# Optimization experiments

Measured on AMD Instinct MI355X. Metric: run time of the kernel, lower is better.

## Reference

```python
import jax, jax.numpy as jnp
import numpy as np

B, S, H, NH = 2, 2048, 768, 12
HD = H // NH
MEM_W = 0.5  # memory_weight
LN_EPS = 1e-5


def setup_inputs() -> dict:
    key = jax.random.key(0)
    ks = jax.random.split(key, 12)
    xav = lambda k: jax.random.uniform(k, (H, H), jnp.float32, -1.0, 1.0) * np.sqrt(6.0 / (H + H))
    return {
        "hidden_states": jax.random.normal(ks[0], (B, S, H), jnp.float32),
        "cross_states": jax.random.normal(ks[1], (B, S, H), jnp.float32),
        "attention_mask": jnp.ones((B, 1, S, S), jnp.int32),
        "memory_tensors": jax.random.normal(ks[2], (2, B, S, H), jnp.float32),
        "dynamic_factor": jax.random.uniform(ks[3], (B, S, 1), jnp.float32),
        "Wq": xav(ks[4]), "bq": jnp.zeros((H,), jnp.float32),
        "Wk": xav(ks[5]), "bk": jnp.zeros((H,), jnp.float32),
        "Wv": xav(ks[6]), "bv": jnp.zeros((H,), jnp.float32),
        "Wo": xav(ks[7]), "bo": jnp.zeros((H,), jnp.float32),
        "gate": jnp.ones((1,), jnp.float32),
        "gate_bias": jnp.zeros((1,), jnp.float32),
        "ln_g": jnp.ones((H,), jnp.float32),
        "ln_b": jnp.zeros((H,), jnp.float32),
    }


def _layernorm(x, g, b):
    mu = jnp.mean(x, axis=-1, keepdims=True)
    var = jnp.mean(jnp.square(x - mu), axis=-1, keepdims=True)
    return (x - mu) * jax.lax.rsqrt(var + LN_EPS) * g + b


def reference(hidden_states, cross_states, attention_mask, memory_tensors,
              dynamic_factor, Wq, bq, Wk, bk, Wv, bv, Wo, bo,
              gate, gate_bias, ln_g, ln_b):
    x = _layernorm(hidden_states, ln_g, ln_b)
    q = x @ Wq + bq                      # [B,S,H]
    k = cross_states @ Wk + bk
    v = cross_states @ Wv + bv
    k = k + memory_tensors[0] * MEM_W    # memory injection into K/V
    v = v + memory_tensors[1] * MEM_W

    q = q.reshape(B, S, NH, HD).transpose(0, 2, 1, 3)  # [B,NH,S,HD]
    k = k.reshape(B, S, NH, HD).transpose(0, 2, 1, 3)
    v = v.reshape(B, S, NH, HD).transpose(0, 2, 1, 3)

    scores = jnp.einsum("bhqd,bhkd->bhqk", q, k) / np.sqrt(HD)
    scores = jnp.where(attention_mask == 0, -jnp.inf, scores)
    attn = jax.nn.softmax(scores, axis=-1)
    out = jnp.einsum("bhqk,bhkd->bhqd", attn, v)       # [B,NH,S,HD]
    out = out.transpose(0, 2, 1, 3).reshape(B, S, H)

    out = out @ Wo + bo
    out = out * gate + gate_bias
    out = out * dynamic_factor
    return out
```

## Files before the change

### kernel.cpp

```cpp
#include <hip/hip_runtime.h>
#include <hip/hip_bf16.h>
#include <stdint.h>

#define BB   2
#define SS   2048
#define HH   768
#define NHH  12
#define HDD  64
#define BSS  (BB*SS)
#define NBH  (BB*NHH)
#define ROWS_BH (NBH*SS)
#define NSPLIT 2

typedef unsigned short u16;
typedef unsigned int   u32;
typedef __attribute__((ext_vector_type(8))) short bf16x8_t;
typedef __attribute__((ext_vector_type(4))) float f32x4;
typedef __attribute__((ext_vector_type(16))) float f32x16;
typedef __attribute__((ext_vector_type(2))) u32   u32x2;
typedef __attribute__((ext_vector_type(4))) u32   u32x4;

#define MFMA16(a, b, c) __builtin_amdgcn_mfma_f32_16x16x32_bf16((a), (b), (c), 0, 0, 0)
#define MFMA32(a, b, c) __builtin_amdgcn_mfma_f32_32x32x16_bf16((a), (b), (c), 0, 0, 0)

__device__ __forceinline__ float b2f(u16 u) {
    u32 x = ((u32)u) << 16; float f; __builtin_memcpy(&f, &x, 4); return f;
}
__device__ __forceinline__ u16 f2b(float f) {
    u32 x; __builtin_memcpy(&x, &f, 4);
    u32 r = x + 0x7fffu + ((x >> 16) & 1u);
    return (u16)(r >> 16);
}
__device__ __forceinline__ u32 cvtpk(float a, float b) {
    u32 r;
    __asm__("v_cvt_pk_bf16_f32 %0, %1, %2" : "=v"(r) : "v"(a), "v"(b));
    return r;
}
__device__ __forceinline__ void async16(const u16* g, u16* l) {
    __builtin_amdgcn_global_load_lds(
        (const __attribute__((address_space(1))) void*)g,
        (__attribute__((address_space(3))) void*)l, 16, 0, 0);
}

__global__ __launch_bounds__(256) void prep_kernel(
    const float* __restrict__ Wq, const float* __restrict__ Wk,
    const float* __restrict__ Wv, const float* __restrict__ Wo,
    u16* __restrict__ Wt,
    const float* __restrict__ hid, const float* __restrict__ cross,
    const float* __restrict__ g, const float* __restrict__ bb,
    u16* __restrict__ xln, u16* __restrict__ crossb,
    const int* __restrict__ mask, u32* __restrict__ bits,
    u32* __restrict__ wrow)
{
    int id = blockIdx.x;
    int t = threadIdx.x;

    if (id < 576) {
        int mat = id / 144, rem = id % 144;
        int by = rem / 12, bx = rem % 12;
        const float* src = (mat == 0) ? Wq : (mat == 1) ? Wk : (mat == 2) ? Wv : Wo;
        u16* dst = Wt + (size_t)mat * 768 * 768;

        __shared__ float sm[64][68];
        int r0 = by * 64, c0 = bx * 64;
        #pragma unroll
        for (int it = 0; it < 4; ++it) {
            int c = t + it * 256;
            int r = c >> 4, sg = c & 15;
            *(float4*)&sm[r][sg * 4] = *(const float4*)&src[(size_t)(r0 + r) * 768 + c0 + sg * 4];
        }
        __syncthreads();
        #pragma unroll
        for (int it = 0; it < 2; ++it) {
            int c = t + it * 256;
            int rr = c >> 3, sg = c & 7;
            u16 tmp[8] __attribute__((aligned(16)));
            #pragma unroll
            for (int j = 0; j < 8; ++j) tmp[j] = f2b(sm[sg * 8 + j][rr]);
            *(u32x4*)&dst[(size_t)(c0 + rr) * 768 + r0 + sg * 8] = *(u32x4*)tmp;
        }
        return;
    }

    if (id < 2624) {
        int lid = id - 576;
        int y = lid >> 10, bx = lid & 1023;
        int wv = t >> 6, lane = t & 63;
        int row = bx * 4 + wv;

        if (y == 1) {
            const float* xr = cross + (size_t)row * 768;
            u16* o = crossb + (size_t)row * 768;
            #pragma unroll
            for (int c = 0; c < 3; ++c) {
                float4 f = *(const float4*)&xr[c * 256 + lane * 4];
                u16 t4[4] __attribute__((aligned(8)));
                t4[0] = f2b(f.x); t4[1] = f2b(f.y); t4[2] = f2b(f.z); t4[3] = f2b(f.w);
                *(u32x2*)&o[c * 256 + lane * 4] = *(u32x2*)t4;
            }
            return;
        }

        const float* xr = hid + (size_t)row * 768;
        float v[12];
        float s = 0.f, s2 = 0.f;
        #pragma unroll
        for (int c = 0; c < 3; ++c) {
            float4 f = *(const float4*)&xr[c * 256 + lane * 4];
            v[c*4+0] = f.x; v[c*4+1] = f.y; v[c*4+2] = f.z; v[c*4+3] = f.w;
            s  += f.x + f.y + f.z + f.w;
            s2 += f.x*f.x + f.y*f.y + f.z*f.z + f.w*f.w;
        }
        #pragma unroll
        for (int off = 1; off < 64; off <<= 1) {
            s  += __shfl_xor(s,  off, 64);
            s2 += __shfl_xor(s2, off, 64);
        }
        float mu  = s  * (1.f / 768.f);
        float var = s2 * (1.f / 768.f) - mu * mu;
        float rs  = 1.f / sqrtf(var + 1e-5f);
        #pragma unroll
        for (int c = 0; c < 3; ++c) {
            float4 gg = *(const float4*)&g [c * 256 + lane * 4];
            float4 bv = *(const float4*)&bb[c * 256 + lane * 4];
            u16 o[4] __attribute__((aligned(8)));
            o[0] = f2b((v[c*4+0] - mu) * rs * gg.x + bv.x);
            o[1] = f2b((v[c*4+1] - mu) * rs * gg.y + bv.y);
            o[2] = f2b((v[c*4+2] - mu) * rs * gg.z + bv.z);
            o[3] = f2b((v[c*4+3] - mu) * rs * gg.w + bv.w);
            *(u32x2*)&xln[(size_t)row * 768 + c * 256 + lane * 4] = *(u32x2*)o;
        }
        return;
    }

    {
        int mid = id - 2624;
        int w = mid * 256 + t;
        const int4* p = (const int4*)(mask + (size_t)w * 32);
        u32 v = 0;
        #pragma unroll
        for (int i = 0; i < 8; ++i) {
            int4 m = p[i];
            v |= ((m.x != 0) ? 1u : 0u) << (4 * i + 0);
            v |= ((m.y != 0) ? 1u : 0u) << (4 * i + 1);
            v |= ((m.z != 0) ? 1u : 0u) << (4 * i + 2);
            v |= ((m.w != 0) ? 1u : 0u) << (4 * i + 3);
        }
        bits[w] = v;
        unsigned long long ball = __ballot(v == 0xffffffffu);
        if ((t & 63) == 0) {
            u32 wr = 0;
            #pragma unroll
            for (int kt = 0; kt < 32; ++kt)
                if (((ball >> (2 * kt)) & 3ull) == 3ull) wr |= (1u << kt);
            wrow[w >> 6] = wr;
        }
    }
}

__device__ __forceinline__ void gemm64_main(const u16* __restrict__ A,
                                            const u16* __restrict__ W,
                                            f32x4 acc[2][4])
{
    __shared__ __attribute__((aligned(16))) u16 AsL[64 * 64];
    __shared__ __attribute__((aligned(16))) u16 BsL[128 * 64];
    int m0 = blockIdx.x * 64, n0 = blockIdx.y * 128;
    int t = threadIdx.x;
    int wv = t >> 6, lane = t & 63, lm = lane & 15, quad = lane >> 4;
    int wr = wv >> 1, wc = wv & 1;

    for (int kt = 0; kt < 768 / 64; ++kt) {
        __syncthreads();
        #pragma unroll
        for (int it = 0; it < 2; ++it) {
            int c = t + it * 256;
            int row = c >> 3, cs = (c & 7) ^ (row & 7);
            async16(A + (size_t)(m0 + row) * 768 + kt * 64 + cs * 8, &AsL[c * 8]);
        }
        #pragma unroll
        for (int it = 0; it < 4; ++it) {
            int c = t + it * 256;
            int row = c >> 3, cs = (c & 7) ^ (row & 7);
            async16(W + (size_t)(n0 + row) * 768 + kt * 64 + cs * 8, &BsL[c * 8]);
        }
        __syncthreads();
        #pragma unroll
        for (int kk = 0; kk < 2; ++kk) {
            bf16x8_t af[2], bfv[4];
            #pragma unroll
            for (int i = 0; i < 2; ++i) {
                int r = wr * 32 + i * 16 + lm;
                af[i] = *(const bf16x8_t*)&AsL[(r * 8 + ((kk * 4 + quad) ^ (r & 7))) * 8];
            }
            #pragma unroll
            for (int j = 0; j < 4; ++j) {
                int r = wc * 64 + j * 16 + lm;
                bfv[j] = *(const bf16x8_t*)&BsL[(r * 8 + ((kk * 4 + quad) ^ (r & 7))) * 8];
            }
            #pragma unroll
            for (int i = 0; i < 2; ++i)
                #pragma unroll
                for (int j = 0; j < 4; ++j)
                    acc[i][j] = MFMA16(af[i], bfv[j], acc[i][j]);
        }
    }
}

__global__ __launch_bounds__(256) void qkv_gemm(
    const u16* __restrict__ xln, const u16* __restrict__ crossb,
    const u16* __restrict__ Wt,  const float* __restrict__ bq,
    const float* __restrict__ bk, const float* __restrict__ bv,
    const float* __restrict__ mem,
    u16* __restrict__ Qb, u16* __restrict__ Kb, u16* __restrict__ VtG)
{
    int z = blockIdx.z;
    const u16* A      = (z == 0) ? xln : crossb;
    const u16* W      = Wt + (size_t)z * 768 * 768;
    const float* bias = (z == 0) ? bq : (z == 1) ? bk : bv;
    const float* mp   = (z == 0) ? (const float*)nullptr : mem + (size_t)(z - 1) * BSS * HH;

    f32x4 z4 = {0.f, 0.f, 0.f, 0.f};
    f32x4 acc[2][4];
    #pragma unroll
    for (int i = 0; i < 2; ++i)
        #pragma unroll
        for (int j = 0; j < 4; ++j) acc[i][j] = z4;

    gemm64_main(A, W, acc);

    int t = threadIdx.x, wv = t >> 6, lane = t & 63, lm = lane & 15, quad = lane >> 4;
    int wr = wv >> 1, wc = wv & 1;
    int row0 = blockIdx.x * 64 + wr * 32 + quad * 4;
    int col0 = blockIdx.y * 128 + wc * 64 + lm;

    if (z == 2) {
        #pragma unroll
        for (int j = 0; j < 4; ++j) {
            int cg = col0 + j * 16;
            float bz = bias[cg];
            int h = cg >> 6, d = cg & 63;
            #pragma unroll
            for (int i = 0; i < 2; ++i) {
                int rg = row0 + i * 16;
                int b = rg >> 11, s = rg & 2047;
                u16 ob[4] __attribute__((aligned(8)));
                #pragma unroll
                for (int e = 0; e < 4; ++e) {
                    float v = acc[i][j][e] + bz + 0.5f * mp[(size_t)(rg + e) * HH + cg];
                    ob[e] = f2b(v);
                }
                *(u32x2*)&VtG[((size_t)(b * NHH + h) * 64 + d) * SS + s] = *(u32x2*)ob;
            }
        }
        return;
    }

    u16* out = (z == 0) ? Qb : Kb;
    #pragma unroll
    for (int j = 0; j < 4; ++j) {
        int cg = col0 + j * 16;
        float bz = bias[cg];
        #pragma unroll
        for (int i = 0; i < 2; ++i) {
            int rg = row0 + i * 16;
            #pragma unroll
            for (int e = 0; e < 4; ++e) {
                float v = acc[i][j][e] + bz;
                if (mp) v += 0.5f * mp[(size_t)(rg + e) * HH + cg];
                out[(size_t)(rg + e) * HH + cg] = f2b(v);
            }
        }
    }
}

__global__ __launch_bounds__(256, 3) void attn_kernel(
    const u16* __restrict__ Q, const u16* __restrict__ K,
    const u16* __restrict__ VtG, const u32* __restrict__ mbits,
    const u32* __restrict__ wrow,
    u16* __restrict__ Pacc, float* __restrict__ Pl, int ksteps)
{
    __shared__ __attribute__((aligned(16))) u16 KsL[2][64 * 64];
    __shared__ __attribute__((aligned(16))) u16 VtL[2][64 * 64];

    int qt = blockIdx.x;
    int bh = blockIdx.y;
    int z  = blockIdx.z;
    int b = bh / NHH, h = bh % NHH;
    int t = threadIdx.x;
    int wv = t >> 6, lane = t & 63;
    int q31 = lane & 31, hi = lane >> 5;

    int qbase = qt * 128 + wv * 32;
    const u16* qp = Q + (size_t)(b * SS + qbase + q31) * HH + h * 64 + hi * 8;
    bf16x8_t qf0 = *(const bf16x8_t*)&qp[0];
    bf16x8_t qf1 = *(const bf16x8_t*)&qp[16];
    bf16x8_t qf2 = *(const bf16x8_t*)&qp[32];
    bf16x8_t qf3 = *(const bf16x8_t*)&qp[48];

    f32x16 acc0 = {};
    f32x16 acc1 = {};
    float l_lane = 0.f;

    const float SC = 0.18033688011112042f;

    u32 wl = wrow[b * SS + qbase + q31];
    const u32* mrow = &mbits[(size_t)(b * SS + qbase + q31) * (SS / 32)];

    int kr = t >> 3, cs = (t & 7) ^ (kr & 7);
    const u16* Kb0 = K + (size_t)(b * SS) * HH + h * 64;
    const u16* Vb0 = VtG + (size_t)bh * 64 * SS;

    auto STAGE = [&](int pp, int kt) {
        int k0 = kt * 64;
        #pragma unroll
        for (int it = 0; it < 2; ++it) {
            int c = t + it * 256;
            int rr = c >> 3, ss = (c & 7) ^ (rr & 7);
            async16(Kb0 + (size_t)(k0 + rr) * HH + ss * 8, &KsL[pp][c * 8]);
            async16(Vb0 + (size_t)rr * SS + k0 + ss * 8,   &VtL[pp][c * 8]);
        }
    };
    (void)kr; (void)cs;

    int kt0 = z * ksteps, ktE = kt0 + ksteps;
    STAGE(0, kt0);
    __syncthreads();

    for (int kt = kt0; kt < ktE; ++kt) {
        int p = (kt - kt0) & 1;
        if (kt + 1 < ktE) STAGE(p ^ 1, kt + 1);

        bool ok = __all((int)((wl >> kt) & 1u));
        unsigned long long mw = ~0ull;
        if (!ok) {
            u32x2 u = *(const u32x2*)&mrow[kt * 2];
            mw = ((unsigned long long)u.y << 32) | (unsigned long long)u.x;
        }

        #pragma unroll
        for (int kb = 0; kb < 2; ++kb) {
            f32x16 sc = {};
            #pragma unroll
            for (int step = 0; step < 4; ++step) {
                int row = kb * 32 + q31;
                int ch = (step * 2 + hi) ^ (row & 7);
                bf16x8_t kf = *(const bf16x8_t*)&KsL[p][(row * 8 + ch) * 8];
                bf16x8_t qf = (step == 0) ? qf0 : (step == 1) ? qf1 : (step == 2) ? qf2 : qf3;
                sc = MFMA32(kf, qf, sc);
            }

            #pragma unroll
            for (int r = 0; r < 16; ++r) {
                float pv = __builtin_amdgcn_exp2f(sc[r] * SC);
                if (!ok) {
                    int kbit = kb * 32 + (r & 3) + 8 * (r >> 2) + 4 * hi;
                    if (!((mw >> kbit) & 1ull)) pv = 0.f;
                }
                sc[r] = pv;
                l_lane += pv;
            }

            #pragma unroll
            for (int s2 = 0; s2 < 2; ++s2) {
                u32 P0 = cvtpk(sc[8 * s2 + 0], sc[8 * s2 + 1]);
                u32 P1 = cvtpk(sc[8 * s2 + 2], sc[8 * s2 + 3]);
                u32 P2 = cvtpk(sc[8 * s2 + 4], sc[8 * s2 + 5]);
                u32 P3 = cvtpk(sc[8 * s2 + 6], sc[8 * s2 + 7]);
                auto s02 = __builtin_amdgcn_permlane32_swap((int)P0, (int)P2, false, false);
                auto s13 = __builtin_amdgcn_permlane32_swap((int)P1, (int)P3, false, false);
                u32x4 w;
                w.x = (u32)s02[0]; w.y = (u32)s13[0];
                w.z = (u32)s02[1]; w.w = (u32)s13[1];
                bf16x8_t pf = __builtin_bit_cast(bf16x8_t, w);

                int vrow0 = q31;
                int vrow1 = 32 + q31;
                int ch = kb * 4 + s2 * 2 + hi;
                bf16x8_t vf0 = *(const bf16x8_t*)&VtL[p][(vrow0 * 8 + (ch ^ (vrow0 & 7))) * 8];
                bf16x8_t vf1 = *(const bf16x8_t*)&VtL[p][(vrow1 * 8 + (ch ^ (vrow1 & 7))) * 8];
                acc0 = MFMA32(pf, vf0, acc0);
                acc1 = MFMA32(pf, vf1, acc1);
            }
        }

        __syncthreads();
    }

    l_lane += __shfl_xor(l_lane, 32, 64);

    size_t prow0 = ((size_t)z * NBH + bh) * SS + qt * 128 + wv * 32;
    #pragma unroll
    for (int r = 0; r < 16; ++r) {
        int qrow = (r & 3) + 8 * (r >> 2) + 4 * hi;
        Pacc[(prow0 + qrow) * 64 + q31]      = f2b(acc0[r]);
        Pacc[(prow0 + qrow) * 64 + 32 + q31] = f2b(acc1[r]);
    }
    if (lane < 32) Pl[prow0 + lane] = l_lane;
}

__global__ __launch_bounds__(256) void attn_merge(
    const u16* __restrict__ Pacc, const float* __restrict__ Pl,
    u16* __restrict__ AO)
{
    int t = threadIdx.x;
    int r = blockIdx.x * 64 + (t >> 2);
    int dseg = (t & 3) * 16;

    float lsum = Pl[r] + Pl[(size_t)ROWS_BH + r];

    float o[16];
    #pragma unroll
    for (int i = 0; i < 16; ++i) o[i] = 0.f;
    #pragma unroll
    for (int s = 0; s < NSPLIT; ++s) {
        const u16* ap = &Pacc[((size_t)s * ROWS_BH + r) * 64 + dseg];
        u32x4 a0 = *(const u32x4*)ap;
        u32x4 a1 = *(const u32x4*)(ap + 8);
        u32 wa[8];
        wa[0]=a0.x; wa[1]=a0.y; wa[2]=a0.z; wa[3]=a0.w;
        wa[4]=a1.x; wa[5]=a1.y; wa[6]=a1.z; wa[7]=a1.w;
        #pragma unroll
        for (int i = 0; i < 8; ++i) {
            o[2*i]   += b2f((u16)(wa[i] & 0xffff));
            o[2*i+1] += b2f((u16)(wa[i] >> 16));
        }
    }
    float inv = 1.f / lsum;
    int bh = r >> 11, q = r & 2047;
    int b = bh / NHH, h = bh % NHH;
    u16 ob[16] __attribute__((aligned(16)));
    #pragma unroll
    for (int i = 0; i < 16; ++i) ob[i] = f2b(o[i] * inv);
    u16* op = &AO[((size_t)(b * SS + q)) * HH + h * 64 + dseg];
    *(u32x4*)op       = *(u32x4*)ob;
    *(u32x4*)(op + 8) = *(u32x4*)(ob + 8);
}

__global__ __launch_bounds__(256) void out_gemm(
    const u16* __restrict__ AO, const u16* __restrict__ Wt,
    const float* __restrict__ bo, const float* __restrict__ gate,
    const float* __restrict__ gbias, const float* __restrict__ dyn,
    float* __restrict__ out)
{
    f32x4 z4 = {0.f, 0.f, 0.f, 0.f};
    f32x4 acc[2][4];
    #pragma unroll
    for (int i = 0; i < 2; ++i)
        #pragma unroll
        for (int j = 0; j < 4; ++j) acc[i][j] = z4;

    gemm64_main(AO, Wt, acc);

    float gv = gate[0];
    float gb = gbias[0];
    int t = threadIdx.x, wv = t >> 6, lane = t & 63, lm = lane & 15, quad = lane >> 4;
    int wr = wv >> 1, wc = wv & 1;
    int row0 = blockIdx.x * 64 + wr * 32 + quad * 4;
    int col0 = blockIdx.y * 128 + wc * 64 + lm;
    #pragma unroll
    for (int j = 0; j < 4; ++j) {
        int cg = col0 + j * 16;
        float bz = bo[cg];
        #pragma unroll
        for (int i = 0; i < 2; ++i) {
            int rg = row0 + i * 16;
            #pragma unroll
            for (int e = 0; e < 4; ++e) {
                float v = acc[i][j][e] + bz;
                v = v * gv + gb;
                v *= dyn[rg + e];
                out[(size_t)(rg + e) * HH + cg] = v;
            }
        }
    }
}

extern "C" void kernel_launch(void* const* d_in, const int* in_sizes, int n_in,
                              void* d_out, int out_size, void* d_ws, size_t ws_size,
                              hipStream_t stream)
{
    (void)in_sizes; (void)n_in; (void)out_size; (void)ws_size;

    const float* hid   = (const float*)d_in[0];
    const float* cross = (const float*)d_in[1];
    const int*   amask = (const int*)d_in[2];
    const float* mem   = (const float*)d_in[3];
    const float* dyn   = (const float*)d_in[4];
    const float* Wq    = (const float*)d_in[5];
    const float* bq    = (const float*)d_in[6];
    const float* Wk    = (const float*)d_in[7];
    const float* bk    = (const float*)d_in[8];
    const float* Wv    = (const float*)d_in[9];
    const float* bv    = (const float*)d_in[10];
    const float* Wo    = (const float*)d_in[11];
    const float* bo    = (const float*)d_in[12];
    const float* gate  = (const float*)d_in[13];
    const float* gbias = (const float*)d_in[14];
    const float* lng   = (const float*)d_in[15];
    const float* lnb   = (const float*)d_in[16];

    char* p = (char*)d_ws;
    u16* Wt   = (u16*)p; p += (size_t)4 * 768 * 768 * 2;
    u32* mb   = (u32*)p; p += (size_t)BB * SS * (SS / 32) * 4;
    u32* wrow = (u32*)p; p += (size_t)BSS * 4;
    u16* xln  = (u16*)p; p += (size_t)BSS * HH * 2;
    u16* crb  = (u16*)p; p += (size_t)BSS * HH * 2;
    u16* Qb   = (u16*)p; p += (size_t)BSS * HH * 2;
    u16* Kb   = (u16*)p; p += (size_t)BSS * HH * 2;
    u16* VtG  = (u16*)p; p += (size_t)BSS * HH * 2;
    u16* Pacc  = xln;
    float* Pl  = (float*)Wt;
    u16* AO    = Kb;

    prep_kernel <<<dim3(3648),           256, 0, stream>>>(
        Wq, Wk, Wv, Wo, Wt, hid, cross, lng, lnb, xln, crb, amask, mb, wrow);
    qkv_gemm    <<<dim3(64, 6, 3),       256, 0, stream>>>(
        xln, crb, Wt, bq, bk, bv, mem, Qb, Kb, VtG);
    attn_kernel <<<dim3(16, 24, NSPLIT), 256, 0, stream>>>(
        Qb, Kb, VtG, mb, wrow, Pacc, Pl, SS / 64 / NSPLIT);
    attn_merge  <<<dim3(ROWS_BH / 64),   256, 0, stream>>>(Pacc, Pl, AO);
    out_gemm    <<<dim3(64, 6),          256, 0, stream>>>(
        AO, Wt + (size_t)3 * 768 * 768, bo, gate, gbias, dyn, (float*)d_out);
}
```

Baseline: 238.7 us.

## Triple-buffer attention K/V loads and remap block IDs for XCD locality

The attention kernel moves from double to triple buffering of K/V tiles. It uses explicit vmcnt waits and a single barrier per step, and the compile-time k-loop is fully unrolled, so loads run two tiles ahead of compute. All three GEMM/attention kernels switch to a 1-D grid with a block-ID swizzle `(bid&7)*N + bid>>3`. This places neighbouring logical tiles on the same XCD to improve L2 reuse. In exchange, LDS per block grows, which may lower occupancy, and the hand-written waitcnt counts depend on how many loads each stage issues.

```diff
diff --git a/kernel.cpp b/kernel.cpp
--- a/kernel.cpp
+++ b/kernel.cpp
@@ -11,6 +11,7 @@
 #define NBH  (BB*NHH)
 #define ROWS_BH (NBH*SS)
 #define NSPLIT 2
+#define KST  (SS / 64 / NSPLIT)
 
 typedef unsigned short u16;
 typedef unsigned int   u32;
@@ -160,11 +161,11 @@
 
 __device__ __forceinline__ void gemm64_main(const u16* __restrict__ A,
                                             const u16* __restrict__ W,
+                                            int m0, int n0,
                                             f32x4 acc[2][4])
 {
     __shared__ __attribute__((aligned(16))) u16 AsL[64 * 64];
     __shared__ __attribute__((aligned(16))) u16 BsL[128 * 64];
-    int m0 = blockIdx.x * 64, n0 = blockIdx.y * 128;
     int t = threadIdx.x;
     int wv = t >> 6, lane = t & 63, lm = lane & 15, quad = lane >> 4;
     int wr = wv >> 1, wc = wv & 1;
@@ -213,7 +214,13 @@
     const float* __restrict__ mem,
     u16* __restrict__ Qb, u16* __restrict__ Kb, u16* __restrict__ VtG)
 {
-    int z = blockIdx.z;
+    int bid = blockIdx.x;
+    int logical = (bid & 7) * 144 + (bid >> 3);
+    int bx = logical & 63;
+    int rest = logical >> 6;
+    int by = rest % 6;
+    int z  = rest / 6;
+
     const u16* A      = (z == 0) ? xln : crossb;
     const u16* W      = Wt + (size_t)z * 768 * 768;
     const float* bias = (z == 0) ? bq : (z == 1) ? bk : bv;
@@ -226,12 +233,12 @@
         #pragma unroll
         for (int j = 0; j < 4; ++j) acc[i][j] = z4;
 
-    gemm64_main(A, W, acc);
+    gemm64_main(A, W, bx * 64, by * 128, acc);
 
     int t = threadIdx.x, wv = t >> 6, lane = t & 63, lm = lane & 15, quad = lane >> 4;
     int wr = wv >> 1, wc = wv & 1;
-    int row0 = blockIdx.x * 64 + wr * 32 + quad * 4;
-    int col0 = blockIdx.y * 128 + wc * 64 + lm;
+    int row0 = bx * 64 + wr * 32 + quad * 4;
+    int col0 = by * 128 + wc * 64 + lm;
 
     if (z == 2) {
         #pragma unroll
@@ -277,14 +284,18 @@
     const u16* __restrict__ Q, const u16* __restrict__ K,
     const u16* __restrict__ VtG, const u32* __restrict__ mbits,
     const u32* __restrict__ wrow,
-    u16* __restrict__ Pacc, float* __restrict__ Pl, int ksteps)
-{
-    __shared__ __attribute__((aligned(16))) u16 KsL[2][64 * 64];
-    __shared__ __attribute__((aligned(16))) u16 VtL[2][64 * 64];
-
-    int qt = blockIdx.x;
-    int bh = blockIdx.y;
-    int z  = blockIdx.z;
+    u16* __restrict__ Pacc, float* __restrict__ Pl)
+{
+    __shared__ __attribute__((aligned(16))) u16 KsL[3][64 * 64];
+    __shared__ __attribute__((aligned(16))) u16 VtL[3][64 * 64];
+
+    int bid = blockIdx.x;
+    int logical = (bid & 7) * 96 + (bid >> 3);
+    int qt = logical & 15;
+    int g  = logical >> 4;
+    int bh = g >> 1;
+    int z  = g & 1;
+
     int b = bh / NHH, h = bh % NHH;
     int t = threadIdx.x;
     int wv = t >> 6, lane = t & 63;
@@ -306,7 +317,6 @@
     u32 wl = wrow[b * SS + qbase + q31];
     const u32* mrow = &mbits[(size_t)(b * SS + qbase + q31) * (SS / 32)];
 
-    int kr = t >> 3, cs = (t & 7) ^ (kr & 7);
     const u16* Kb0 = K + (size_t)(b * SS) * HH + h * 64;
     const u16* Vb0 = VtG + (size_t)bh * 64 * SS;
 
@@ -320,15 +330,25 @@
             async16(Vb0 + (size_t)rr * SS + k0 + ss * 8,   &VtL[pp][c * 8]);
         }
     };
-    (void)kr; (void)cs;
-
-    int kt0 = z * ksteps, ktE = kt0 + ksteps;
+
+    int kt0 = z * KST;
     STAGE(0, kt0);
-    __syncthreads();
-
-    for (int kt = kt0; kt < ktE; ++kt) {
-        int p = (kt - kt0) & 1;
-        if (kt + 1 < ktE) STAGE(p ^ 1, kt + 1);
+    __builtin_amdgcn_sched_barrier(0);
+    STAGE(1, kt0 + 1);
+    __builtin_amdgcn_sched_barrier(0);
+
+    #pragma unroll
+    for (int i = 0; i < KST; ++i) {
+        int kt = kt0 + i;
+        int cur = i % 3;
+
+        if (i + 1 < KST) { __asm__ volatile("s_waitcnt vmcnt(4)" ::: "memory"); }
+        else             { __asm__ volatile("s_waitcnt vmcnt(0)" ::: "memory"); }
+        __builtin_amdgcn_s_barrier();
+        __builtin_amdgcn_sched_barrier(0);
+
+        if (i + 2 < KST) STAGE((i + 2) % 3, kt + 2);
+        __builtin_amdgcn_sched_barrier(0);
 
         bool ok = __all((int)((wl >> kt) & 1u));
         unsigned long long mw = ~0ull;
@@ -344,7 +364,7 @@
             for (int step = 0; step < 4; ++step) {
                 int row = kb * 32 + q31;
                 int ch = (step * 2 + hi) ^ (row & 7);
-                bf16x8_t kf = *(const bf16x8_t*)&KsL[p][(row * 8 + ch) * 8];
+                bf16x8_t kf = *(const bf16x8_t*)&KsL[cur][(row * 8 + ch) * 8];
                 bf16x8_t qf = (step == 0) ? qf0 : (step == 1) ? qf1 : (step == 2) ? qf2 : qf3;
                 sc = MFMA32(kf, qf, sc);
             }
@@ -376,14 +396,12 @@
                 int vrow0 = q31;
                 int vrow1 = 32 + q31;
                 int ch = kb * 4 + s2 * 2 + hi;
-                bf16x8_t vf0 = *(const bf16x8_t*)&VtL[p][(vrow0 * 8 + (ch ^ (vrow0 & 7))) * 8];
-                bf16x8_t vf1 = *(const bf16x8_t*)&VtL[p][(vrow1 * 8 + (ch ^ (vrow1 & 7))) * 8];
+                bf16x8_t vf0 = *(const bf16x8_t*)&VtL[cur][(vrow0 * 8 + (ch ^ (vrow0 & 7))) * 8];
+                bf16x8_t vf1 = *(const bf16x8_t*)&VtL[cur][(vrow1 * 8 + (ch ^ (vrow1 & 7))) * 8];
                 acc0 = MFMA32(pf, vf0, acc0);
                 acc1 = MFMA32(pf, vf1, acc1);
             }
         }
-
-        __syncthreads();
     }
 
     l_lane += __shfl_xor(l_lane, 32, 64);
@@ -442,6 +460,11 @@
     const float* __restrict__ gbias, const float* __restrict__ dyn,
     float* __restrict__ out)
 {
+    int bid = blockIdx.x;
+    int logical = (bid & 7) * 48 + (bid >> 3);
+    int bx = logical % 64;
+    int by = logical / 64;
+
     f32x4 z4 = {0.f, 0.f, 0.f, 0.f};
     f32x4 acc[2][4];
     #pragma unroll
@@ -449,14 +472,14 @@
         #pragma unroll
         for (int j = 0; j < 4; ++j) acc[i][j] = z4;
 
-    gemm64_main(AO, Wt, acc);
+    gemm64_main(AO, Wt, bx * 64, by * 128, acc);
 
     float gv = gate[0];
     float gb = gbias[0];
     int t = threadIdx.x, wv = t >> 6, lane = t & 63, lm = lane & 15, quad = lane >> 4;
     int wr = wv >> 1, wc = wv & 1;
-    int row0 = blockIdx.x * 64 + wr * 32 + quad * 4;
-    int col0 = blockIdx.y * 128 + wc * 64 + lm;
+    int row0 = bx * 64 + wr * 32 + quad * 4;
+    int col0 = by * 128 + wc * 64 + lm;
     #pragma unroll
     for (int j = 0; j < 4; ++j) {
         int cg = col0 + j * 16;
@@ -512,13 +535,13 @@
     float* Pl  = (float*)Wt;
     u16* AO    = Kb;
 
-    prep_kernel <<<dim3(3648),           256, 0, stream>>>(
+    prep_kernel <<<dim3(3648),         256, 0, stream>>>(
         Wq, Wk, Wv, Wo, Wt, hid, cross, lng, lnb, xln, crb, amask, mb, wrow);
-    qkv_gemm    <<<dim3(64, 6, 3),       256, 0, stream>>>(
+    qkv_gemm    <<<dim3(1152),         256, 0, stream>>>(
         xln, crb, Wt, bq, bk, bv, mem, Qb, Kb, VtG);
-    attn_kernel <<<dim3(16, 24, NSPLIT), 256, 0, stream>>>(
-        Qb, Kb, VtG, mb, wrow, Pacc, Pl, SS / 64 / NSPLIT);
-    attn_merge  <<<dim3(ROWS_BH / 64),   256, 0, stream>>>(Pacc, Pl, AO);
-    out_gemm    <<<dim3(64, 6),          256, 0, stream>>>(
+    attn_kernel <<<dim3(768),          256, 0, stream>>>(
+        Qb, Kb, VtG, mb, wrow, Pacc, Pl);
+    attn_merge  <<<dim3(ROWS_BH / 64), 256, 0, stream>>>(Pacc, Pl, AO);
+    out_gemm    <<<dim3(384),          256, 0, stream>>>(
         AO, Wt + (size_t)3 * 768 * 768, bo, gate, gbias, dyn, (float*)d_out);
 }
```

Result: slower. 518.8 us (+117.3%).

## Fuse split-K attention merge into output projection GEMM A-tile loads

Applied to the files above, without the earlier changes.

Removes the separate attn_merge kernel. The output GEMM now reads the two split-K partial accumulators and row sums directly, normalizes them and converts to bf16 while filling its shared-memory A tile. This saves one kernel launch and the write and read-back of the intermediate attention-output buffer. In exchange, each of the six column blocks redoes the merge for its rows and reads both partial buffers. The inlined K loop is also a single-buffered, synchronous loader, which may lose overlap compared with the previous shared GEMM routine.

```diff
diff --git a/kernel.cpp b/kernel.cpp
--- a/kernel.cpp
+++ b/kernel.cpp
@@ -306,7 +306,6 @@
     u32 wl = wrow[b * SS + qbase + q31];
     const u32* mrow = &mbits[(size_t)(b * SS + qbase + q31) * (SS / 32)];
 
-    int kr = t >> 3, cs = (t & 7) ^ (kr & 7);
     const u16* Kb0 = K + (size_t)(b * SS) * HH + h * 64;
     const u16* Vb0 = VtG + (size_t)bh * 64 * SS;
 
@@ -320,7 +319,6 @@
             async16(Vb0 + (size_t)rr * SS + k0 + ss * 8,   &VtL[pp][c * 8]);
         }
     };
-    (void)kr; (void)cs;
 
     int kt0 = z * ksteps, ktE = kt0 + ksteps;
     STAGE(0, kt0);
@@ -398,50 +396,16 @@
     if (lane < 32) Pl[prow0 + lane] = l_lane;
 }
 
-__global__ __launch_bounds__(256) void attn_merge(
+__global__ __launch_bounds__(256) void out_gemm(
     const u16* __restrict__ Pacc, const float* __restrict__ Pl,
-    u16* __restrict__ AO)
-{
-    int t = threadIdx.x;
-    int r = blockIdx.x * 64 + (t >> 2);
-    int dseg = (t & 3) * 16;
-
-    float lsum = Pl[r] + Pl[(size_t)ROWS_BH + r];
-
-    float o[16];
-    #pragma unroll
-    for (int i = 0; i < 16; ++i) o[i] = 0.f;
-    #pragma unroll
-    for (int s = 0; s < NSPLIT; ++s) {
-        const u16* ap = &Pacc[((size_t)s * ROWS_BH + r) * 64 + dseg];
-        u32x4 a0 = *(const u32x4*)ap;
-        u32x4 a1 = *(const u32x4*)(ap + 8);
-        u32 wa[8];
-        wa[0]=a0.x; wa[1]=a0.y; wa[2]=a0.z; wa[3]=a0.w;
-        wa[4]=a1.x; wa[5]=a1.y; wa[6]=a1.z; wa[7]=a1.w;
-        #pragma unroll
-        for (int i = 0; i < 8; ++i) {
-            o[2*i]   += b2f((u16)(wa[i] & 0xffff));
-            o[2*i+1] += b2f((u16)(wa[i] >> 16));
-        }
-    }
-    float inv = 1.f / lsum;
-    int bh = r >> 11, q = r & 2047;
-    int b = bh / NHH, h = bh % NHH;
-    u16 ob[16] __attribute__((aligned(16)));
-    #pragma unroll
-    for (int i = 0; i < 16; ++i) ob[i] = f2b(o[i] * inv);
-    u16* op = &AO[((size_t)(b * SS + q)) * HH + h * 64 + dseg];
-    *(u32x4*)op       = *(u32x4*)ob;
-    *(u32x4*)(op + 8) = *(u32x4*)(ob + 8);
-}
-
-__global__ __launch_bounds__(256) void out_gemm(
-    const u16* __restrict__ AO, const u16* __restrict__ Wt,
+    const u16* __restrict__ Wt,
     const float* __restrict__ bo, const float* __restrict__ gate,
     const float* __restrict__ gbias, const float* __restrict__ dyn,
     float* __restrict__ out)
 {
+    __shared__ __attribute__((aligned(16))) u16 AsL[64 * 64];
+    __shared__ __attribute__((aligned(16))) u16 BsL[128 * 64];
+
     f32x4 z4 = {0.f, 0.f, 0.f, 0.f};
     f32x4 acc[2][4];
     #pragma unroll
@@ -449,12 +413,66 @@
         #pragma unroll
         for (int j = 0; j < 4; ++j) acc[i][j] = z4;
 
-    gemm64_main(AO, Wt, acc);
+    int m0 = blockIdx.x * 64, n0 = blockIdx.y * 128;
+    int t = threadIdx.x;
+    int wv = t >> 6, lane = t & 63, lm = lane & 15, quad = lane >> 4;
+    int wr = wv >> 1, wc = wv & 1;
+
+    for (int kt = 0; kt < 768 / 64; ++kt) {
+        __syncthreads();
+        #pragma unroll
+        for (int it = 0; it < 4; ++it) {
+            int c = t + it * 256;
+            int row = c >> 3, cs = (c & 7) ^ (row & 7);
+            async16(Wt + (size_t)(n0 + row) * 768 + kt * 64 + cs * 8, &BsL[c * 8]);
+        }
+        #pragma unroll
+        for (int it = 0; it < 2; ++it) {
+            int c = t + it * 256;
+            int row = c >> 3, cs = (c & 7) ^ (row & 7);
+            int gr = m0 + row;
+            int b = gr >> 11, s = gr & 2047;
+            size_t r0 = ((size_t)(b * NHH + kt)) * SS + s;
+            size_t r1 = r0 + (size_t)NBH * SS;
+            float inv = 1.f / (Pl[r0] + Pl[r1]);
+            u32x4 a0 = *(const u32x4*)&Pacc[r0 * 64 + cs * 8];
+            u32x4 a1 = *(const u32x4*)&Pacc[r1 * 64 + cs * 8];
+            u32 w0[4] = {a0.x, a0.y, a0.z, a0.w};
+            u32 w1[4] = {a1.x, a1.y, a1.z, a1.w};
+            u16 ob[8] __attribute__((aligned(16)));
+            #pragma unroll
+            for (int j = 0; j < 4; ++j) {
+                float lo = (b2f((u16)(w0[j] & 0xffff)) + b2f((u16)(w1[j] & 0xffff))) * inv;
+                float hi = (b2f((u16)(w0[j] >> 16))    + b2f((u16)(w1[j] >> 16)))    * inv;
+                ob[2 * j]     = f2b(lo);
+                ob[2 * j + 1] = f2b(hi);
+            }
+            *(u32x4*)&AsL[c * 8] = *(u32x4*)ob;
+        }
+        __syncthreads();
+        #pragma unroll
+        for (int kk = 0; kk < 2; ++kk) {
+            bf16x8_t af[2], bfv[4];
+            #pragma unroll
+            for (int i = 0; i < 2; ++i) {
+                int r = wr * 32 + i * 16 + lm;
+                af[i] = *(const bf16x8_t*)&AsL[(r * 8 + ((kk * 4 + quad) ^ (r & 7))) * 8];
+            }
+            #pragma unroll
+            for (int j = 0; j < 4; ++j) {
+                int r = wc * 64 + j * 16 + lm;
+                bfv[j] = *(const bf16x8_t*)&BsL[(r * 8 + ((kk * 4 + quad) ^ (r & 7))) * 8];
+            }
+            #pragma unroll
+            for (int i = 0; i < 2; ++i)
+                #pragma unroll
+                for (int j = 0; j < 4; ++j)
+                    acc[i][j] = MFMA16(af[i], bfv[j], acc[i][j]);
+        }
+    }
 
     float gv = gate[0];
     float gb = gbias[0];
-    int t = threadIdx.x, wv = t >> 6, lane = t & 63, lm = lane & 15, quad = lane >> 4;
-    int wr = wv >> 1, wc = wv & 1;
     int row0 = blockIdx.x * 64 + wr * 32 + quad * 4;
     int col0 = blockIdx.y * 128 + wc * 64 + lm;
     #pragma unroll
@@ -510,7 +528,6 @@
     u16* VtG  = (u16*)p; p += (size_t)BSS * HH * 2;
     u16* Pacc  = xln;
     float* Pl  = (float*)Wt;
-    u16* AO    = Kb;
 
     prep_kernel <<<dim3(3648),           256, 0, stream>>>(
         Wq, Wk, Wv, Wo, Wt, hid, cross, lng, lnb, xln, crb, amask, mb, wrow);
@@ -518,7 +535,6 @@
         xln, crb, Wt, bq, bk, bv, mem, Qb, Kb, VtG);
     attn_kernel <<<dim3(16, 24, NSPLIT), 256, 0, stream>>>(
         Qb, Kb, VtG, mb, wrow, Pacc, Pl, SS / 64 / NSPLIT);
-    attn_merge  <<<dim3(ROWS_BH / 64),   256, 0, stream>>>(Pacc, Pl, AO);
     out_gemm    <<<dim3(64, 6),          256, 0, stream>>>(
-        AO, Wt + (size_t)3 * 768 * 768, bo, gate, gbias, dyn, (float*)d_out);
-}
+        Pacc, Pl, Wt + (size_t)3 * 768 * 768, bo, gate, gbias, dyn, (float*)d_out);
+}
```

New measurement: 246.0 us. 3.1% more time.
